# Kernel tuning notes

Measured on AMD Instinct MI355X. Metric: run time of the kernel, lower is better.

The kernel has to match this reference:

```python
import jax, jax.numpy as jnp
import numpy as np

T_FRAMES = 8
N_HEADS = 8
N_GROUPS = 32
EPS = 1e-5


def _group_norm(x, w, b):
    # x: (N, C, L); GroupNorm with 32 groups over (C//32, L)
    N, C, L = x.shape
    xg = x.reshape(N, N_GROUPS, -1)
    m = xg.mean(-1, keepdims=True)
    v = xg.var(-1, keepdims=True)
    xg = (xg - m) / jnp.sqrt(v + EPS)
    return xg.reshape(N, C, L) * w[None, :, None] + b[None, :, None]


def _layer_norm(x, w, b):
    m = x.mean(-1, keepdims=True)
    v = x.var(-1, keepdims=True)
    return (x - m) / jnp.sqrt(v + EPS) * w + b


def _cross_attn(v, l, qw, qb, kw, kb, vw, vb, ow, ob):
    # v: (B, Tq, v_dim), l: (B, Tk, l_dim); weights torch-style (out, in)
    B, Tq, _ = v.shape
    E = qw.shape[0]
    hd = E // N_HEADS
    def split(t):
        return t.reshape(B, -1, N_HEADS, hd).transpose(0, 2, 1, 3)
    q = split((v @ qw.T + qb) * (hd ** -0.5))
    k = split(l @ kw.T + kb)
    val = split(l @ vw.T + vb)
    aw = jnp.einsum('bhqd,bhkd->bhqk', q, k)
    aw = jnp.clip(aw - jnp.max(aw), -50000.0, 50000.0)  # stable_softmax_2d + clamps
    p = jax.nn.softmax(aw, axis=-1)
    o = jnp.einsum('bhqk,bhkd->bhqd', p, val)
    return o.transpose(0, 2, 1, 3).reshape(B, Tq, E) @ ow.T + ob


def _block(v, l, lnvw, lnvb, lnlw, lnlb, qw, qb, kw, kb, vw, vb, ow, ob, gamma):
    # CrossAttentionBlock: residual is on the NORMALIZED v (as in the torch code)
    vn = _layer_norm(v, lnvw, lnvb)
    ln_ = _layer_norm(l, lnlw, lnlb)
    return vn + gamma * _cross_attn(vn, ln_, qw, qb, kw, kb, vw, vb, ow, ob)


def _forward(x, context, gn1_w, gn1_b, gn2_w, gn2_b,
             sa_lnv_w, sa_lnv_b, sa_lnl_w, sa_lnl_b,
             sa_qw, sa_qb, sa_kw, sa_kb, sa_vw, sa_vb, sa_ow, sa_ob, sa_gamma,
             ca_lnv_w, ca_lnv_b, ca_lnl_w, ca_lnl_b,
             ca_qw, ca_qb, ca_kw, ca_kb, ca_vw, ca_vb, ca_ow, ca_ob, ca_gamma):
    BT, C, H, W = x.shape
    T = T_FRAMES
    B = BT // T
    HW = H * W
    # '(b f) c x y -> b c f x y' then 'b c f x y -> (b f) c (x y)' is identity up to flattening spatial
    xn = _group_norm(x.reshape(BT, C, HW), gn1_w, gn1_b)
    xs = xn.reshape(B, T, C, HW).transpose(0, 1, 3, 2)  # (b, f, hw, c)
    outs = []
    for idx in range(T):
        # window_mask row idx has ones at frames [max(0, idx-1), idx]
        frames = np.array([0]) if idx == 0 else np.array([idx - 1, idx])
        xa = xs[:, frames]                                   # (b, nf, hw, c)
        # rearrange 'b f l d -> b (l f) d' : token-major interleave of gathered frames
        xa = xa.transpose(0, 2, 1, 3).reshape(B, HW * frames.shape[0], C)
        outs.append(_block(xs[:, idx], xa,
                           sa_lnv_w, sa_lnv_b, sa_lnl_w, sa_lnl_b,
                           sa_qw, sa_qb, sa_kw, sa_kb, sa_vw, sa_vb, sa_ow, sa_ob, sa_gamma))
    xs = jnp.stack(outs, axis=1) + xs
    xn2 = xs.transpose(0, 1, 3, 2).reshape(BT, C, HW)
    v = _group_norm(xn2, gn2_w, gn2_b).transpose(0, 2, 1)    # ((b f), hw, c)
    ctx = jnp.tile(context, (T, 1, 1))                        # torch .repeat(f,1,1)
    v = _block(v, ctx,
               ca_lnv_w, ca_lnv_b, ca_lnl_w, ca_lnl_b,
               ca_qw, ca_qb, ca_kw, ca_kb, ca_vw, ca_vb, ca_ow, ca_ob, ca_gamma)
    return v.transpose(0, 2, 1).reshape(BT, C, H, W)


def setup_inputs() -> dict:
    key = jax.random.key(0)
    C, LANG, T, B, H, W, NTXT = 512, 512, 8, 2, 32, 32, 77
    ks = jax.random.split(key, 16)
    def lin(k, o, i):
        return jax.random.normal(k, (o, i), jnp.float32) * 0.02
    inp = {
        'x': jax.random.normal(ks[0], (B * T, C, H, W), jnp.float32),
        'context': jax.random.normal(ks[1], (B, NTXT, LANG), jnp.float32),
        'gn1_w': jnp.ones((C,), jnp.float32), 'gn1_b': jnp.zeros((C,), jnp.float32),
        'gn2_w': jnp.ones((C,), jnp.float32), 'gn2_b': jnp.zeros((C,), jnp.float32),
        'sa_lnv_w': jnp.ones((C,), jnp.float32), 'sa_lnv_b': jnp.zeros((C,), jnp.float32),
        'sa_lnl_w': jnp.ones((C,), jnp.float32), 'sa_lnl_b': jnp.zeros((C,), jnp.float32),
        'sa_qw': lin(ks[2], C, C), 'sa_qb': jnp.zeros((C,), jnp.float32),
        'sa_kw': lin(ks[3], C, C), 'sa_kb': jnp.zeros((C,), jnp.float32),
        'sa_vw': lin(ks[4], C, C), 'sa_vb': jnp.zeros((C,), jnp.float32),
        'sa_ow': lin(ks[5], C, C), 'sa_ob': jnp.zeros((C,), jnp.float32),
        'sa_gamma': jnp.full((C,), 1e-4, jnp.float32),
        'ca_lnv_w': jnp.ones((C,), jnp.float32), 'ca_lnv_b': jnp.zeros((C,), jnp.float32),
        'ca_lnl_w': jnp.ones((LANG,), jnp.float32), 'ca_lnl_b': jnp.zeros((LANG,), jnp.float32),
        'ca_qw': lin(ks[6], C, C), 'ca_qb': jnp.zeros((C,), jnp.float32),
        'ca_kw': lin(ks[7], C, LANG), 'ca_kb': jnp.zeros((C,), jnp.float32),
        'ca_vw': lin(ks[8], C, LANG), 'ca_vb': jnp.zeros((C,), jnp.float32),
        'ca_ow': lin(ks[9], C, C), 'ca_ob': jnp.zeros((C,), jnp.float32),
        'ca_gamma': jnp.full((C,), 1e-4, jnp.float32),
    }
    return inp


def reference(x, context, gn1_w, gn1_b, gn2_w, gn2_b,
              sa_lnv_w, sa_lnv_b, sa_lnl_w, sa_lnl_b,
              sa_qw, sa_qb, sa_kw, sa_kb, sa_vw, sa_vb, sa_ow, sa_ob, sa_gamma,
              ca_lnv_w, ca_lnv_b, ca_lnl_w, ca_lnl_b,
              ca_qw, ca_qb, ca_kw, ca_kb, ca_vw, ca_vb, ca_ow, ca_ob, ca_gamma):
    return _forward(x, context, gn1_w, gn1_b, gn2_w, gn2_b,
                    sa_lnv_w, sa_lnv_b, sa_lnl_w, sa_lnl_b,
                    sa_qw, sa_qb, sa_kw, sa_kb, sa_vw, sa_vb, sa_ow, sa_ob, sa_gamma,
                    ca_lnv_w, ca_lnv_b, ca_lnl_w, ca_lnl_b,
                    ca_qw, ca_qb, ca_kw, ca_kb, ca_vw, ca_vb, ca_ow, ca_ob, ca_gamma)
```

## Files before the change

kernel.cpp:

```cpp
#include <hip/hip_runtime.h>

typedef __attribute__((ext_vector_type(8))) short short8;
typedef __attribute__((ext_vector_type(4))) short short4v;
typedef __attribute__((ext_vector_type(4))) float floatx4;

#define MFMA_BF16 __builtin_amdgcn_mfma_f32_16x16x32_bf16
#define LOG2E 1.44269504088896340736f

__device__ inline floatx4 MFMA16(short4v a, short4v b, floatx4 c){
#if defined(__HIP_DEVICE_COMPILE__)
  return __builtin_amdgcn_mfma_f32_16x16x16bf16_1k(a, b, c, 0, 0, 0);
#else
  return c;
#endif
}

__device__ inline void gll16(const unsigned short* g, unsigned short* l){
#if defined(__HIP_DEVICE_COMPILE__)
  __builtin_amdgcn_global_load_lds(
      (const __attribute__((address_space(1))) unsigned int*)g,
      (__attribute__((address_space(3))) unsigned int*)l, 16, 0, 0);
#else
  (void)g; (void)l;
#endif
}

__device__ inline unsigned short f2bf(float x){
  unsigned int u = __float_as_uint(x);
  u += 0x7fffu + ((u >> 16) & 1u);
  return (unsigned short)(u >> 16);
}
__device__ inline unsigned pack_bf(float lo, float hi){
  return __builtin_amdgcn_perm(__float_as_uint(hi), __float_as_uint(lo), 0x07060302u);
}

__device__ inline float wave_sum(float v){
  #pragma unroll
  for(int m=32;m>=1;m>>=1) v += __shfl_xor(v,m);
  return v;
}

__global__ __launch_bounds__(256) void gn1_kernel(const float* __restrict__ x,
    const float* __restrict__ w, const float* __restrict__ b, float* __restrict__ xs){
  int g = blockIdx.x, bt = blockIdx.y, tid = threadIdx.x;
  const float* xp = x + ((size_t)bt*512 + g*16)*1024;
  float s=0.f, s2=0.f;
  #pragma unroll
  for(int it=0; it<16; ++it){
    float4 v = *(const float4*)(xp + it*1024 + tid*4);
    s  += v.x+v.y+v.z+v.w;
    s2 += v.x*v.x+v.y*v.y+v.z*v.z+v.w*v.w;
  }
  __shared__ float red[8];
  s = wave_sum(s); s2 = wave_sum(s2);
  int wid = tid>>6;
  if((tid&63)==0){ red[wid*2]=s; red[wid*2+1]=s2; }
  __syncthreads();
  s  = red[0]+red[2]+red[4]+red[6];
  s2 = red[1]+red[3]+red[5]+red[7];
  float mean = s * (1.f/16384.f);
  float var  = s2 * (1.f/16384.f) - mean*mean;
  float rinv = rsqrtf(var + 1e-5f);
  int c = tid & 15, h0 = tid >> 4;
  float sc = w[g*16+c]*rinv;
  float sh = b[g*16+c] - mean*sc;
  const float* xcol = xp + (size_t)c*1024;
  float* op = xs + (size_t)bt*1024*512 + g*16 + c;
  #pragma unroll 4
  for(int it=0; it<64; ++it){
    int hw = h0 + it*16;
    op[(size_t)hw*512] = xcol[hw]*sc + sh;
  }
}

__global__ __launch_bounds__(256) void ln_dual_kernel(const float* __restrict__ xs,
    const float* __restrict__ lvw, const float* __restrict__ lvb,
    const float* __restrict__ llw, const float* __restrict__ llb,
    float* __restrict__ vn, unsigned short* __restrict__ vnb, unsigned short* __restrict__ lnlb){
  int wid = threadIdx.x>>6, l = threadIdx.x&63;
  size_t row = (size_t)blockIdx.x*4 + wid;
  const float* xp = xs + row*512;
  float4 a = *(const float4*)(xp + l*4);
  float4 c = *(const float4*)(xp + 256 + l*4);
  float s  = a.x+a.y+a.z+a.w + c.x+c.y+c.z+c.w;
  float s2 = a.x*a.x+a.y*a.y+a.z*a.z+a.w*a.w + c.x*c.x+c.y*c.y+c.z*c.z+c.w*c.w;
  s = wave_sum(s); s2 = wave_sum(s2);
  float mean = s*(1.f/512.f);
  float rinv = rsqrtf(s2*(1.f/512.f) - mean*mean + 1e-5f);
  int c0 = l*4, c1 = 256 + l*4;
  float y[8] = {(a.x-mean)*rinv,(a.y-mean)*rinv,(a.z-mean)*rinv,(a.w-mean)*rinv,
                (c.x-mean)*rinv,(c.y-mean)*rinv,(c.z-mean)*rinv,(c.w-mean)*rinv};
  float4 o0, o1;
  o0.x=y[0]*lvw[c0+0]+lvb[c0+0]; o0.y=y[1]*lvw[c0+1]+lvb[c0+1];
  o0.z=y[2]*lvw[c0+2]+lvb[c0+2]; o0.w=y[3]*lvw[c0+3]+lvb[c0+3];
  o1.x=y[4]*lvw[c1+0]+lvb[c1+0]; o1.y=y[5]*lvw[c1+1]+lvb[c1+1];
  o1.z=y[6]*lvw[c1+2]+lvb[c1+2]; o1.w=y[7]*lvw[c1+3]+lvb[c1+3];
  *(float4*)(vn + row*512 + c0) = o0;
  *(float4*)(vn + row*512 + c1) = o1;
  ushort4 h;
  h.x=f2bf(o0.x); h.y=f2bf(o0.y); h.z=f2bf(o0.z); h.w=f2bf(o0.w);
  *(ushort4*)(vnb + row*512 + c0) = h;
  h.x=f2bf(o1.x); h.y=f2bf(o1.y); h.z=f2bf(o1.z); h.w=f2bf(o1.w);
  *(ushort4*)(vnb + row*512 + c1) = h;
  h.x=f2bf(y[0]*llw[c0+0]+llb[c0+0]); h.y=f2bf(y[1]*llw[c0+1]+llb[c0+1]);
  h.z=f2bf(y[2]*llw[c0+2]+llb[c0+2]); h.w=f2bf(y[3]*llw[c0+3]+llb[c0+3]);
  *(ushort4*)(lnlb + row*512 + c0) = h;
  h.x=f2bf(y[4]*llw[c1+0]+llb[c1+0]); h.y=f2bf(y[5]*llw[c1+1]+llb[c1+1]);
  h.z=f2bf(y[6]*llw[c1+2]+llb[c1+2]); h.w=f2bf(y[7]*llw[c1+3]+llb[c1+3]);
  *(ushort4*)(lnlb + row*512 + c1) = h;
}

__global__ __launch_bounds__(256) void gn2ln_kernel(const float* __restrict__ xs2, const float* __restrict__ st,
    const float* __restrict__ gw, const float* __restrict__ gb,
    const float* __restrict__ lw, const float* __restrict__ lb,
    float* __restrict__ vn2, unsigned short* __restrict__ vn2b){
  int wid = threadIdx.x>>6, l = threadIdx.x&63;
  size_t row = (size_t)blockIdx.x*4 + wid;
  int bt = (int)(row >> 10);
  const float* xp = xs2 + row*512;
  float4 a = *(const float4*)(xp + l*4);
  float4 c = *(const float4*)(xp + 256 + l*4);
  int c0 = l*4, c1 = 256 + l*4;
  int g0 = c0>>4, g1 = c1>>4;
  float sm0 = st[(bt*32+g0)*2], sq0 = st[(bt*32+g0)*2+1];
  float sm1 = st[(bt*32+g1)*2], sq1 = st[(bt*32+g1)*2+1];
  float m0 = sm0*(1.f/16384.f);
  float r0 = rsqrtf(sq0*(1.f/16384.f) - m0*m0 + 1e-5f);
  float m1 = sm1*(1.f/16384.f);
  float r1 = rsqrtf(sq1*(1.f/16384.f) - m1*m1 + 1e-5f);
  float y[8];
  y[0]=(a.x-m0)*r0*gw[c0+0]+gb[c0+0]; y[1]=(a.y-m0)*r0*gw[c0+1]+gb[c0+1];
  y[2]=(a.z-m0)*r0*gw[c0+2]+gb[c0+2]; y[3]=(a.w-m0)*r0*gw[c0+3]+gb[c0+3];
  y[4]=(c.x-m1)*r1*gw[c1+0]+gb[c1+0]; y[5]=(c.y-m1)*r1*gw[c1+1]+gb[c1+1];
  y[6]=(c.z-m1)*r1*gw[c1+2]+gb[c1+2]; y[7]=(c.w-m1)*r1*gw[c1+3]+gb[c1+3];
  float s=0.f, s2=0.f;
  #pragma unroll
  for(int i=0;i<8;++i){ s += y[i]; s2 += y[i]*y[i]; }
  s = wave_sum(s); s2 = wave_sum(s2);
  float mean = s*(1.f/512.f);
  float rinv = rsqrtf(s2*(1.f/512.f) - mean*mean + 1e-5f);
  float4 o0, o1;
  o0.x=(y[0]-mean)*rinv*lw[c0+0]+lb[c0+0]; o0.y=(y[1]-mean)*rinv*lw[c0+1]+lb[c0+1];
  o0.z=(y[2]-mean)*rinv*lw[c0+2]+lb[c0+2]; o0.w=(y[3]-mean)*rinv*lw[c0+3]+lb[c0+3];
  o1.x=(y[4]-mean)*rinv*lw[c1+0]+lb[c1+0]; o1.y=(y[5]-mean)*rinv*lw[c1+1]+lb[c1+1];
  o1.z=(y[6]-mean)*rinv*lw[c1+2]+lb[c1+2]; o1.w=(y[7]-mean)*rinv*lw[c1+3]+lb[c1+3];
  *(float4*)(vn2 + row*512 + c0) = o0;
  *(float4*)(vn2 + row*512 + c1) = o1;
  ushort4 h;
  h.x=f2bf(o0.x); h.y=f2bf(o0.y); h.z=f2bf(o0.z); h.w=f2bf(o0.w);
  *(ushort4*)(vn2b + row*512 + c0) = h;
  h.x=f2bf(o1.x); h.y=f2bf(o1.y); h.z=f2bf(o1.z); h.w=f2bf(o1.w);
  *(ushort4*)(vn2b + row*512 + c1) = h;
}

__global__ __launch_bounds__(256) void ctxln_kernel(const float* __restrict__ ctx,
    const float* __restrict__ lw, const float* __restrict__ lb, unsigned short* __restrict__ out){
  int wid = threadIdx.x>>6, l = threadIdx.x&63;
  int row = blockIdx.x*4 + wid;
  if(row >= 154) return;
  const float* xp = ctx + (size_t)row*512;
  float4 a = *(const float4*)(xp + l*4);
  float4 c = *(const float4*)(xp + 256 + l*4);
  float s  = a.x+a.y+a.z+a.w + c.x+c.y+c.z+c.w;
  float s2 = a.x*a.x+a.y*a.y+a.z*a.z+a.w*a.w + c.x*c.x+c.y*c.y+c.z*c.z+c.w*c.w;
  s = wave_sum(s); s2 = wave_sum(s2);
  float mean = s*(1.f/512.f);
  float rinv = rsqrtf(s2*(1.f/512.f) - mean*mean + 1e-5f);
  int c0 = l*4, c1 = 256 + l*4;
  ushort4 h;
  h.x=f2bf((a.x-mean)*rinv*lw[c0+0]+lb[c0+0]); h.y=f2bf((a.y-mean)*rinv*lw[c0+1]+lb[c0+1]);
  h.z=f2bf((a.z-mean)*rinv*lw[c0+2]+lb[c0+2]); h.w=f2bf((a.w-mean)*rinv*lw[c0+3]+lb[c0+3]);
  *(ushort4*)(out + (size_t)row*512 + c0) = h;
  h.x=f2bf((c.x-mean)*rinv*lw[c1+0]+lb[c1+0]); h.y=f2bf((c.y-mean)*rinv*lw[c1+1]+lb[c1+1]);
  h.z=f2bf((c.z-mean)*rinv*lw[c1+2]+lb[c1+2]); h.w=f2bf((c.w-mean)*rinv*lw[c1+3]+lb[c1+3]);
  *(ushort4*)(out + (size_t)row*512 + c1) = h;
}

__global__ __launch_bounds__(256) void cvtw_kernel(const float* s0, const float* s1, const float* s2,
    const float* s3, const float* s4, const float* s5, const float* s6, const float* s7,
    unsigned short* __restrict__ dst){
  const float* srcs[8] = {s0,s1,s2,s3,s4,s5,s6,s7};
  int w = blockIdx.y;
  const float* src = srcs[w];
  int i = (blockIdx.x*256 + threadIdx.x)*4;
  float4 v = *(const float4*)(src + i);
  ushort4 h; h.x=f2bf(v.x); h.y=f2bf(v.y); h.z=f2bf(v.z); h.w=f2bf(v.w);
  *(ushort4*)(dst + (size_t)w*262144 + i) = h;
}

template<int MODE>
__global__ __launch_bounds__(256) void gemm128_kernel(const unsigned short* __restrict__ A,
    const unsigned short* __restrict__ W, const float* __restrict__ bias, int M, float scale,
    unsigned short* __restrict__ outb, float* __restrict__ outf,
    const float* __restrict__ r1, const float* __restrict__ r2, const float* __restrict__ gamma){
  __shared__ unsigned short Asl[2][128*64];
  __shared__ unsigned short Wsl[2][128*64];
  int tid = threadIdx.x, l = tid&63, wid = tid>>6, quad = l>>4, ln16 = l&15;
  int wr = wid>>1, wc = wid&1;
  int m0 = blockIdx.x*128, n0 = blockIdx.y*128;
  const unsigned short* Ag[4];
  const unsigned short* Wg[4];
  unsigned short* Al[4];
  unsigned short* Wl[4];
  #pragma unroll
  for(int i=0;i<4;++i){
    int s = i*256 + tid;
    int row = s>>3, kg = s&7;
    int kgs = kg ^ (row&7);
    int ar = m0+row; if(ar > M-1) ar = M-1;
    Ag[i] = A + (size_t)ar*512 + kgs*8;
    Wg[i] = W + (size_t)(n0+row)*512 + kgs*8;
    Al[i] = &Asl[0][0] + row*64 + kg*8;
    Wl[i] = &Wsl[0][0] + row*64 + kg*8;
  }
  floatx4 acc[4][4];
  #pragma unroll
  for(int mf=0;mf<4;++mf)
    #pragma unroll
    for(int nf=0;nf<4;++nf) acc[mf][nf] = (floatx4){0,0,0,0};
  #pragma unroll
  for(int i=0;i<4;++i){ gll16(Ag[i], Al[i]); gll16(Wg[i], Wl[i]); }
  for(int kt=0; kt<8; ++kt){
    int cur = kt&1;
    if(kt<7){
      int k0n = (kt+1)*64, off = (cur^1)*8192;
      #pragma unroll
      for(int i=0;i<4;++i){ gll16(Ag[i]+k0n, Al[i]+off); gll16(Wg[i]+k0n, Wl[i]+off); }
      asm volatile("s_waitcnt vmcnt(8)" ::: "memory");
    } else {
      asm volatile("s_waitcnt vmcnt(0)" ::: "memory");
    }
    __builtin_amdgcn_s_barrier();
    __builtin_amdgcn_sched_barrier(0);
    const unsigned short* Ab = &Asl[cur][0];
    const unsigned short* Wbb = &Wsl[cur][0];
    #pragma unroll
    for(int kk=0; kk<2; ++kk){
      short8 av[4], wv[4];
      #pragma unroll
      for(int mf=0;mf<4;++mf){
        int row = wr*64 + mf*16 + ln16;
        int sread = (kk*4 + quad) ^ (row&7);
        av[mf] = *(const short8*)(Ab + row*64 + sread*8);
      }
      #pragma unroll
      for(int nf=0;nf<4;++nf){
        int row = wc*64 + nf*16 + ln16;
        int sread = (kk*4 + quad) ^ (row&7);
        wv[nf] = *(const short8*)(Wbb + row*64 + sread*8);
      }
      #pragma unroll
      for(int mf=0;mf<4;++mf)
        #pragma unroll
        for(int nf=0;nf<4;++nf)
          acc[mf][nf] = MFMA_BF16(av[mf], wv[nf], acc[mf][nf], 0,0,0);
    }
    if(kt<7){
      __builtin_amdgcn_sched_barrier(0);
      __builtin_amdgcn_s_barrier();
    }
  }
  if(MODE==1){
    float gs[4]={0,0,0,0}, gs2[4]={0,0,0,0};
    #pragma unroll
    for(int mf=0;mf<4;++mf){
      int mb = m0 + wr*64 + mf*16 + quad*4;
      #pragma unroll
      for(int nf=0;nf<4;++nf){
        int col = n0 + wc*64 + nf*16 + ln16;
        float bv = bias[col];
        float gv = gamma[col];
        #pragma unroll
        for(int r=0;r<4;++r){
          size_t ix = (size_t)(mb+r)*512 + col;
          float val = r1[ix] + r2[ix] + gv*(acc[mf][nf][r] + bv);
          outf[ix] = val;
          gs[nf] += val; gs2[nf] += val*val;
        }
      }
    }
    float* stats = (float*)outb;
    int btq = m0 >> 10;
    #pragma unroll
    for(int nf=0;nf<4;++nf){
      float sv  = wave_sum(gs[nf]);
      float sv2 = wave_sum(gs2[nf]);
      if(l==0){
        int g = (n0 + wc*64 + nf*16) >> 4;
        atomicAdd(&stats[(btq*32+g)*2],   sv);
        atomicAdd(&stats[(btq*32+g)*2+1], sv2);
      }
    }
    return;
  }
  #pragma unroll
  for(int mf=0;mf<4;++mf){
    int mb = m0 + wr*64 + mf*16 + quad*4;
    #pragma unroll
    for(int nf=0;nf<4;++nf){
      int col = n0 + wc*64 + nf*16 + ln16;
      float bv = bias[col];
      if(MODE==0){
        #pragma unroll
        for(int r=0;r<4;++r){
          int m = mb + r;
          if(m < M) outb[(size_t)m*512 + col] = f2bf((acc[mf][nf][r] + bv)*scale);
        }
      } else if(MODE==2){
        float gv = gamma[col];
        int bt = mb >> 10;
        int hw0 = mb & 1023;
        float4 ov;
        ov.x = r1[(size_t)(mb+0)*512+col] + gv*(acc[mf][nf][0]+bv);
        ov.y = r1[(size_t)(mb+1)*512+col] + gv*(acc[mf][nf][1]+bv);
        ov.z = r1[(size_t)(mb+2)*512+col] + gv*(acc[mf][nf][2]+bv);
        ov.w = r1[(size_t)(mb+3)*512+col] + gv*(acc[mf][nf][3]+bv);
        *(float4*)(outf + (size_t)bt*524288 + (size_t)col*1024 + hw0) = ov;
      } else if(MODE==3){
        int bf = mb >> 10;
        int hw0 = mb & 1023;
        ushort4 h;
        h.x = f2bf(acc[mf][nf][0]+bv); h.y = f2bf(acc[mf][nf][1]+bv);
        h.z = f2bf(acc[mf][nf][2]+bv); h.w = f2bf(acc[mf][nf][3]+bv);
        *(ushort4*)(outb + ((size_t)bf*512 + col)*1024 + hw0) = h;
      } else if(MODE==4){
        #pragma unroll
        for(int r=0;r<4;++r){
          int m = mb + r;
          if(m < M){
            int cb = (m >= 77) ? 1 : 0;
            int key = m - 77*cb;
            outb[((size_t)cb*512 + col)*128 + key] = f2bf(acc[mf][nf][r] + bv);
          }
        }
      }
    }
  }
}

__global__ __launch_bounds__(256, 2) void attn_sp_kernel(const unsigned short* __restrict__ Q,
    const unsigned short* __restrict__ K, const unsigned short* __restrict__ VT,
    unsigned short* __restrict__ O){
  int id = blockIdx.x;
  int hb = id & 127, qt = id >> 7;
  int head = hb >> 4, bz = hb & 15;
  int b = bz >> 3, idx = bz & 7;
  int tid = threadIdx.x, wid = tid>>6, l = tid&63, quad = l>>4, ln16 = l&15;
  __shared__ unsigned short vt[2][64*72];
  __shared__ unsigned short kt[2][64*72];
  size_t qbase = (size_t)bz*1024 + qt*256 + wid*64 + ln16;
  short8 qb[4][2];
  #pragma unroll
  for(int grp=0;grp<4;++grp){
    const unsigned short* qp = Q + (qbase + grp*16)*512 + head*64 + quad*8;
    qb[grp][0] = *(const short8*)(qp);
    qb[grp][1] = *(const short8*)(qp + 32);
  }
  floatx4 o[4][4];
  #pragma unroll
  for(int g=0;g<4;++g)
    #pragma unroll
    for(int d=0;d<4;++d) o[g][d] = (floatx4){0,0,0,0};
  float lr[4] = {0.f,0.f,0.f,0.f};
  int nch = idx ? 32 : 16;
  int f0  = idx ? (idx-1) : 0;
  int sr = tid>>2, sc0 = (tid&3)*16;
  short8 pv0, pv1, pk0, pk1;
  {
    const unsigned short* vp = VT + (((size_t)(b*8+f0)*512) + head*64 + sr)*1024 + sc0;
    pv0 = *(const short8*)(vp); pv1 = *(const short8*)(vp + 8);
    const unsigned short* kp = K + (((size_t)(b*8+f0))*1024 + sr)*512 + head*64 + sc0;
    pk0 = *(const short8*)(kp); pk1 = *(const short8*)(kp + 8);
  }
  for(int ch=0; ch<nch; ++ch){
    int bf_ = ch & 1;
    *(short8*)(&vt[bf_][0] + sr*72 + sc0)     = pv0;
    *(short8*)(&vt[bf_][0] + sr*72 + sc0 + 8) = pv1;
    *(short8*)(&kt[bf_][0] + sr*72 + sc0)     = pk0;
    *(short8*)(&kt[bf_][0] + sr*72 + sc0 + 8) = pk1;
    if(ch+1 < nch){
      int f = f0 + ((ch+1)>>4);
      int kk0 = ((ch+1)&15)*64;
      const unsigned short* vp = VT + (((size_t)(b*8+f)*512) + head*64 + sr)*1024 + kk0 + sc0;
      pv0 = *(const short8*)(vp); pv1 = *(const short8*)(vp + 8);
      const unsigned short* kp = K + (((size_t)(b*8+f))*1024 + kk0 + sr)*512 + head*64 + sc0;
      pk0 = *(const short8*)(kp); pk1 = *(const short8*)(kp + 8);
    }
    __syncthreads();
    #pragma unroll
    for(int g=0; g<4; ++g){
      const unsigned short* kr = &kt[bf_][0] + (g*16+ln16)*72 + quad*8;
      short8 k0 = *(const short8*)(kr);
      short8 k1 = *(const short8*)(kr + 32);
      short4v va[4];
      #pragma unroll
      for(int dc=0; dc<4; ++dc)
        va[dc] = *(const short4v*)(&vt[bf_][0] + (dc*16+ln16)*72 + g*16 + quad*4);
      #pragma unroll
      for(int grp=0; grp<4; ++grp){
        floatx4 s = {0,0,0,0};
        s = MFMA_BF16(k0, qb[grp][0], s, 0,0,0);
        s = MFMA_BF16(k1, qb[grp][1], s, 0,0,0);
        float p0 = __builtin_amdgcn_exp2f(s[0]);
        float p1 = __builtin_amdgcn_exp2f(s[1]);
        float p2 = __builtin_amdgcn_exp2f(s[2]);
        float p3 = __builtin_amdgcn_exp2f(s[3]);
        lr[grp] += (p0+p1)+(p2+p3);
        uint2 pu; pu.x = pack_bf(p0,p1); pu.y = pack_bf(p2,p3);
        short4v pb = __builtin_bit_cast(short4v, pu);
        #pragma unroll
        for(int dc=0; dc<4; ++dc)
          o[grp][dc] = MFMA16(va[dc], pb, o[grp][dc]);
      }
    }
  }
  #pragma unroll
  for(int grp=0; grp<4; ++grp){
    float lt = lr[grp];
    lt += __shfl_xor(lt, 16); lt += __shfl_xor(lt, 32);
    float inv = __builtin_amdgcn_rcpf(lt);
    size_t orow = qbase + grp*16;
    unsigned short* op = O + orow*512 + head*64 + quad*4;
    #pragma unroll
    for(int dc=0; dc<4; ++dc){
      uint2 pk;
      pk.x = pack_bf(o[grp][dc][0]*inv, o[grp][dc][1]*inv);
      pk.y = pack_bf(o[grp][dc][2]*inv, o[grp][dc][3]*inv);
      *(uint2*)(op + dc*16) = pk;
    }
  }
}

__global__ __launch_bounds__(256) void attn_ca_kernel(const unsigned short* __restrict__ Q,
    const unsigned short* __restrict__ K2, const unsigned short* __restrict__ V2T,
    unsigned short* __restrict__ O){
  int id = blockIdx.x;
  int hb = id & 127, qt = id >> 7;
  int head = hb >> 4, bt = hb & 15;
  int cb = bt & 1;
  int tid = threadIdx.x, wid = tid>>6, l = tid&63, quad = l>>4, ln16 = l&15;
  __shared__ unsigned short vt[2][64*72];
  __shared__ unsigned short kt[2][64*72];
  size_t qbase = (size_t)bt*1024 + qt*128 + wid*32 + ln16;
  short8 qb[2][2];
  #pragma unroll
  for(int grp=0;grp<2;++grp){
    const unsigned short* qp = Q + (qbase + grp*16)*512 + head*64 + quad*8;
    qb[grp][0] = *(const short8*)(qp);
    qb[grp][1] = *(const short8*)(qp + 32);
  }
  floatx4 o[2][4];
  #pragma unroll
  for(int g=0;g<2;++g)
    #pragma unroll
    for(int d=0;d<4;++d) o[g][d] = (floatx4){0,0,0,0};
  float lr[2] = {0.f,0.f};
  int sr = tid>>2, sc0 = (tid&3)*16;
  short8 pv0, pv1, pk0, pk1;
  {
    const unsigned short* vp = V2T + (((size_t)cb*512) + head*64 + sr)*128 + sc0;
    pv0 = *(const short8*)(vp); pv1 = *(const short8*)(vp + 8);
    const unsigned short* kp = K2 + ((size_t)cb*77 + sr)*512 + head*64 + sc0;
    pk0 = *(const short8*)(kp); pk1 = *(const short8*)(kp + 8);
  }
  for(int ch=0; ch<2; ++ch){
    int bf_ = ch & 1;
    int kk0 = ch*64;
    *(short8*)(&vt[bf_][0] + sr*72 + sc0)     = pv0;
    *(short8*)(&vt[bf_][0] + sr*72 + sc0 + 8) = pv1;
    *(short8*)(&kt[bf_][0] + sr*72 + sc0)     = pk0;
    *(short8*)(&kt[bf_][0] + sr*72 + sc0 + 8) = pk1;
    if(ch == 0){
      const unsigned short* vp = V2T + (((size_t)cb*512) + head*64 + sr)*128 + 64 + sc0;
      pv0 = *(const short8*)(vp); pv1 = *(const short8*)(vp + 8);
      const unsigned short* kp = K2 + ((size_t)cb*77 + 64 + sr)*512 + head*64 + sc0;
      pk0 = *(const short8*)(kp); pk1 = *(const short8*)(kp + 8);
    }
    __syncthreads();
    #pragma unroll
    for(int g=0; g<4; ++g){
      int kg = kk0 + g*16 + quad*4;
      const unsigned short* kr = &kt[bf_][0] + (g*16+ln16)*72 + quad*8;
      short8 k0 = *(const short8*)(kr);
      short8 k1 = *(const short8*)(kr + 32);
      short4v va[4];
      #pragma unroll
      for(int dc=0; dc<4; ++dc)
        va[dc] = *(const short4v*)(&vt[bf_][0] + (dc*16+ln16)*72 + g*16 + quad*4);
      #pragma unroll
      for(int grp=0; grp<2; ++grp){
        floatx4 s = {0,0,0,0};
        s = MFMA_BF16(k0, qb[grp][0], s, 0,0,0);
        s = MFMA_BF16(k1, qb[grp][1], s, 0,0,0);
        float p0 = (kg+0 < 77) ? __builtin_amdgcn_exp2f(s[0]) : 0.f;
        float p1 = (kg+1 < 77) ? __builtin_amdgcn_exp2f(s[1]) : 0.f;
        float p2 = (kg+2 < 77) ? __builtin_amdgcn_exp2f(s[2]) : 0.f;
        float p3 = (kg+3 < 77) ? __builtin_amdgcn_exp2f(s[3]) : 0.f;
        lr[grp] += (p0+p1)+(p2+p3);
        uint2 pu; pu.x = pack_bf(p0,p1); pu.y = pack_bf(p2,p3);
        short4v pb = __builtin_bit_cast(short4v, pu);
        #pragma unroll
        for(int dc=0; dc<4; ++dc)
          o[grp][dc] = MFMA16(va[dc], pb, o[grp][dc]);
      }
    }
  }
  #pragma unroll
  for(int grp=0; grp<2; ++grp){
    float lt = lr[grp];
    lt += __shfl_xor(lt, 16); lt += __shfl_xor(lt, 32);
    float inv = __builtin_amdgcn_rcpf(lt);
    size_t orow = qbase + grp*16;
    unsigned short* op = O + orow*512 + head*64 + quad*4;
    #pragma unroll
    for(int dc=0; dc<4; ++dc){
      uint2 pk;
      pk.x = pack_bf(o[grp][dc][0]*inv, o[grp][dc][1]*inv);
      pk.y = pack_bf(o[grp][dc][2]*inv, o[grp][dc][3]*inv);
      *(uint2*)(op + dc*16) = pk;
    }
  }
}

extern "C" void kernel_launch(void* const* d_in, const int* in_sizes, int n_in,
                              void* d_out, int out_size, void* d_ws, size_t ws_size,
                              hipStream_t stream) {
  const float* x        = (const float*)d_in[0];
  const float* ctx      = (const float*)d_in[1];
  const float* gn1w     = (const float*)d_in[2];
  const float* gn1b     = (const float*)d_in[3];
  const float* gn2w     = (const float*)d_in[4];
  const float* gn2b     = (const float*)d_in[5];
  const float* sa_lnv_w = (const float*)d_in[6];
  const float* sa_lnv_b = (const float*)d_in[7];
  const float* sa_lnl_w = (const float*)d_in[8];
  const float* sa_lnl_b = (const float*)d_in[9];
  const float* sa_qw    = (const float*)d_in[10];
  const float* sa_qb    = (const float*)d_in[11];
  const float* sa_kw    = (const float*)d_in[12];
  const float* sa_kb    = (const float*)d_in[13];
  const float* sa_vw    = (const float*)d_in[14];
  const float* sa_vb    = (const float*)d_in[15];
  const float* sa_ow    = (const float*)d_in[16];
  const float* sa_ob    = (const float*)d_in[17];
  const float* sa_gamma = (const float*)d_in[18];
  const float* ca_lnv_w = (const float*)d_in[19];
  const float* ca_lnv_b = (const float*)d_in[20];
  const float* ca_lnl_w = (const float*)d_in[21];
  const float* ca_lnl_b = (const float*)d_in[22];
  const float* ca_qw    = (const float*)d_in[23];
  const float* ca_qb    = (const float*)d_in[24];
  const float* ca_kw    = (const float*)d_in[25];
  const float* ca_kb    = (const float*)d_in[26];
  const float* ca_vw    = (const float*)d_in[27];
  const float* ca_vb    = (const float*)d_in[28];
  const float* ca_ow    = (const float*)d_in[29];
  const float* ca_ob    = (const float*)d_in[30];
  const float* ca_gamma = (const float*)d_in[31];

  const size_t BIGF = (size_t)16384*512*4;
  const size_t BIGH = (size_t)16384*512*2;
  char* w8 = (char*)d_ws;
  float*          xs   = (float*)(w8);
  float*          vn   = (float*)(w8 + BIGF);
  unsigned short* vnb  = (unsigned short*)(w8 + 2*BIGF);
  unsigned short* lnlb = (unsigned short*)(w8 + 2*BIGF + 1*BIGH);
  unsigned short* Qb   = (unsigned short*)(w8 + 2*BIGF + 2*BIGH);
  unsigned short* Kb   = (unsigned short*)(w8 + 2*BIGF + 3*BIGH);
  unsigned short* VTb  = (unsigned short*)(w8 + 2*BIGF + 4*BIGH);
  unsigned short* Ob   = (unsigned short*)(w8 + 2*BIGF + 5*BIGH);
  char* small = w8 + 2*BIGF + 6*BIGH;
  float*          st   = (float*)(small);
  unsigned short* ctxb = (unsigned short*)(small + 4096);
  unsigned short* Wb   = (unsigned short*)(small + 4096 + 157696);
  unsigned short* K2b  = (unsigned short*)(w8);
  unsigned short* V2T  = (unsigned short*)(w8 + 1048576);
  float* xs2 = (float*)d_out;

  const float QS = 0.125f * LOG2E;

  cvtw_kernel<<<dim3(256,8),256,0,stream>>>(sa_qw, sa_kw, sa_vw, sa_ow, ca_qw, ca_kw, ca_vw, ca_ow, Wb);
  gn1_kernel<<<dim3(32,16),256,0,stream>>>(x, gn1w, gn1b, xs);
  ln_dual_kernel<<<4096,256,0,stream>>>(xs, sa_lnv_w, sa_lnv_b, sa_lnl_w, sa_lnl_b, vn, vnb, lnlb);
  gemm128_kernel<0><<<dim3(128,4),256,0,stream>>>(vnb,  Wb+0*262144, sa_qb, 16384, QS,   Qb, nullptr, nullptr, nullptr, nullptr);
  gemm128_kernel<0><<<dim3(128,4),256,0,stream>>>(lnlb, Wb+1*262144, sa_kb, 16384, 1.0f, Kb, nullptr, nullptr, nullptr, nullptr);
  gemm128_kernel<3><<<dim3(128,4),256,0,stream>>>(lnlb, Wb+2*262144, sa_vb, 16384, 1.0f, VTb, nullptr, nullptr, nullptr, nullptr);
  attn_sp_kernel<<<512,256,0,stream>>>(Qb, Kb, VTb, Ob);
  (void)hipMemsetAsync(st, 0, 4096, stream);
  gemm128_kernel<1><<<dim3(128,4),256,0,stream>>>(Ob, Wb+3*262144, sa_ob, 16384, 1.0f, (unsigned short*)st, xs2, xs, vn, sa_gamma);
  gn2ln_kernel<<<4096,256,0,stream>>>(xs2, st, gn2w, gn2b, ca_lnv_w, ca_lnv_b, vn, vnb);
  ctxln_kernel<<<39,256,0,stream>>>(ctx, ca_lnl_w, ca_lnl_b, ctxb);
  gemm128_kernel<0><<<dim3(2,4),256,0,stream>>>(ctxb, Wb+5*262144, ca_kb, 154, 1.0f, K2b, nullptr, nullptr, nullptr, nullptr);
  (void)hipMemsetAsync(V2T, 0, (size_t)2*512*128*2, stream);
  gemm128_kernel<4><<<dim3(2,4),256,0,stream>>>(ctxb, Wb+6*262144, ca_vb, 154, 1.0f, V2T, nullptr, nullptr, nullptr, nullptr);
  gemm128_kernel<0><<<dim3(128,4),256,0,stream>>>(vnb, Wb+4*262144, ca_qb, 16384, QS, Qb, nullptr, nullptr, nullptr, nullptr);
  attn_ca_kernel<<<1024,256,0,stream>>>(Qb, K2b, V2T, Ob);
  gemm128_kernel<2><<<dim3(128,4),256,0,stream>>>(Ob, Wb+7*262144, ca_ob, 16384, 1.0f, nullptr, (float*)d_out, vn, nullptr, ca_gamma);
}
```

Before: 431.8 us.

## Stream K/V tiles into LDS via global_load_lds with XOR swizzle

Replaces the register-staged K/V prefetch (global load to registers, then LDS store) in the sparse attention kernel with direct global-to-LDS async loads, double-buffered with explicit vmcnt waits and raw barriers. The padded 72-stride LDS layout becomes an unpadded 64-stride layout with an XOR swizzle on 16-byte chunks to avoid bank conflicts. This aims to free VGPRs and VALU store instructions and to overlap the next tile's fetch with the current tile's MFMA work. It adds an extra barrier per chunk and depends on the hand-written waitcnt values being correct.

```diff
diff --git a/kernel.cpp b/kernel.cpp
--- a/kernel.cpp
+++ b/kernel.cpp
@@ -346,8 +346,8 @@
   int head = hb >> 4, bz = hb & 15;
   int b = bz >> 3, idx = bz & 7;
   int tid = threadIdx.x, wid = tid>>6, l = tid&63, quad = l>>4, ln16 = l&15;
-  __shared__ unsigned short vt[2][64*72];
-  __shared__ unsigned short kt[2][64*72];
+  __shared__ unsigned short kt[2][64*64];
+  __shared__ unsigned short vt[2][64*64];
   size_t qbase = (size_t)bz*1024 + qt*256 + wid*64 + ln16;
   short8 qb[4][2];
   #pragma unroll
@@ -364,38 +364,58 @@
   float lr[4] = {0.f,0.f,0.f,0.f};
   int nch = idx ? 32 : 16;
   int f0  = idx ? (idx-1) : 0;
-  int sr = tid>>2, sc0 = (tid&3)*16;
-  short8 pv0, pv1, pk0, pk1;
+  const unsigned short* Kg[2];
+  const unsigned short* Vg[2];
+  unsigned short* Kl[2];
+  unsigned short* Vl[2];
+  #pragma unroll
+  for(int i=0;i<2;++i){
+    int s = i*256 + tid;
+    int r = s>>3, kg = s&7;
+    int kgs = kg ^ (r&7);
+    Kg[i] = K  + ((size_t)b*8*1024 + r)*512 + head*64 + kgs*8;
+    Vg[i] = VT + ((size_t)b*8*512 + head*64 + r)*1024 + kgs*8;
+    Kl[i] = &kt[0][0] + s*8;
+    Vl[i] = &vt[0][0] + s*8;
+  }
   {
-    const unsigned short* vp = VT + (((size_t)(b*8+f0)*512) + head*64 + sr)*1024 + sc0;
-    pv0 = *(const short8*)(vp); pv1 = *(const short8*)(vp + 8);
-    const unsigned short* kp = K + (((size_t)(b*8+f0))*1024 + sr)*512 + head*64 + sc0;
-    pk0 = *(const short8*)(kp); pk1 = *(const short8*)(kp + 8);
-  }
+    size_t koff = (size_t)f0*1024*512;
+    size_t voff = (size_t)f0*524288;
+    gll16(Kg[0]+koff, Kl[0]); gll16(Kg[1]+koff, Kl[1]);
+    gll16(Vg[0]+voff, Vl[0]); gll16(Vg[1]+voff, Vl[1]);
+  }
+  int sw = ln16 & 7;
   for(int ch=0; ch<nch; ++ch){
     int bf_ = ch & 1;
-    *(short8*)(&vt[bf_][0] + sr*72 + sc0)     = pv0;
-    *(short8*)(&vt[bf_][0] + sr*72 + sc0 + 8) = pv1;
-    *(short8*)(&kt[bf_][0] + sr*72 + sc0)     = pk0;
-    *(short8*)(&kt[bf_][0] + sr*72 + sc0 + 8) = pk1;
     if(ch+1 < nch){
       int f = f0 + ((ch+1)>>4);
       int kk0 = ((ch+1)&15)*64;
-      const unsigned short* vp = VT + (((size_t)(b*8+f)*512) + head*64 + sr)*1024 + kk0 + sc0;
-      pv0 = *(const short8*)(vp); pv1 = *(const short8*)(vp + 8);
-      const unsigned short* kp = K + (((size_t)(b*8+f))*1024 + kk0 + sr)*512 + head*64 + sc0;
-      pk0 = *(const short8*)(kp); pk1 = *(const short8*)(kp + 8);
-    }
-    __syncthreads();
+      size_t koff = ((size_t)f*1024 + kk0)*512;
+      size_t voff = (size_t)f*524288 + kk0;
+      int lo = (bf_^1)*4096;
+      gll16(Kg[0]+koff, Kl[0]+lo); gll16(Kg[1]+koff, Kl[1]+lo);
+      gll16(Vg[0]+voff, Vl[0]+lo); gll16(Vg[1]+voff, Vl[1]+lo);
+      asm volatile("s_waitcnt vmcnt(4)" ::: "memory");
+    } else {
+      asm volatile("s_waitcnt vmcnt(0)" ::: "memory");
+    }
+    __builtin_amdgcn_s_barrier();
+    __builtin_amdgcn_sched_barrier(0);
+    const unsigned short* ktb = &kt[bf_][0];
+    const unsigned short* vtb = &vt[bf_][0];
     #pragma unroll
     for(int g=0; g<4; ++g){
-      const unsigned short* kr = &kt[bf_][0] + (g*16+ln16)*72 + quad*8;
-      short8 k0 = *(const short8*)(kr);
-      short8 k1 = *(const short8*)(kr + 32);
+      int krow = g*16 + ln16;
+      short8 k0 = *(const short8*)(ktb + krow*64 + ((quad  )^sw)*8);
+      short8 k1 = *(const short8*)(ktb + krow*64 + ((quad+4)^sw)*8);
       short4v va[4];
-      #pragma unroll
-      for(int dc=0; dc<4; ++dc)
-        va[dc] = *(const short4v*)(&vt[bf_][0] + (dc*16+ln16)*72 + g*16 + quad*4);
+      int sl = g*2 + (quad>>1);
+      int hh = (quad&1)*4;
+      #pragma unroll
+      for(int dc=0; dc<4; ++dc){
+        int vrow = dc*16 + ln16;
+        va[dc] = *(const short4v*)(vtb + vrow*64 + ((sl^sw)*8) + hh);
+      }
       #pragma unroll
       for(int grp=0; grp<4; ++grp){
         floatx4 s = {0,0,0,0};
@@ -412,6 +432,10 @@
         for(int dc=0; dc<4; ++dc)
           o[grp][dc] = MFMA16(va[dc], pb, o[grp][dc]);
       }
+    }
+    if(ch+1 < nch){
+      __builtin_amdgcn_sched_barrier(0);
+      __builtin_amdgcn_s_barrier();
     }
   }
   #pragma unroll
```

Result: no change. 436.4 us (+1.0%).
